# Performance work log

Measured on AMD Instinct MI355X. Metric: run time of the kernel, lower is better.

## Reference

```python
import jax, jax.numpy as jnp
import numpy as np

B, S, D = 2, 1024, 768
H, HD = 12, 64
E, K, F = 8, 2, 3072
EPS = 1e-5


def _ln(x, g, b):
    mu = jnp.mean(x, -1, keepdims=True)
    var = jnp.mean(jnp.square(x - mu), -1, keepdims=True)
    return (x - mu) * jax.lax.rsqrt(var + EPS) * g + b


def setup_inputs() -> dict:
    key = jax.random.key(0)
    ks = jax.random.split(key, 12)
    s = lambda k, shape, sc: jax.random.normal(k, shape, jnp.float32) * sc
    return {
        "hidden_states": s(ks[0], (B, S, D), 1.0),
        "ln1_g": jnp.ones((D,), jnp.float32), "ln1_b": jnp.zeros((D,), jnp.float32),
        "w_attn": s(ks[1], (D, 3 * D), 0.02), "b_attn": jnp.zeros((3 * D,), jnp.float32),
        "w_attnproj": s(ks[2], (D, D), 0.02), "b_attnproj": jnp.zeros((D,), jnp.float32),
        "ln2_g": jnp.ones((D,), jnp.float32), "ln2_b": jnp.zeros((D,), jnp.float32),
        "w_router": s(ks[3], (E, D), 0.01),
        "w_fc": s(ks[4], (E, D, F), 0.02 / E), "b_fc": jnp.zeros((E, F), jnp.float32),
        "w_proj": s(ks[5], (E, F, D), 0.02 / E), "b_proj": jnp.zeros((E, D), jnp.float32),
    }


def reference(hidden_states, ln1_g, ln1_b, w_attn, b_attn, w_attnproj, b_attnproj,
              ln2_g, ln2_b, w_router, w_fc, b_fc, w_proj, b_proj):
    # --- attention sub-block (GPT-2 style, causal) ---
    residual = hidden_states
    x = _ln(hidden_states, ln1_g, ln1_b)
    qkv = x @ w_attn + b_attn                         # [B,S,3D]
    q, k, v = jnp.split(qkv, 3, axis=-1)
    def heads(t):
        return t.reshape(B, S, H, HD).transpose(0, 2, 1, 3)  # [B,H,S,HD]
    q, k, v = heads(q), heads(k), heads(v)
    scores = jnp.einsum("bhqd,bhkd->bhqk", q, k) / np.sqrt(HD).astype(np.float32)
    causal = jnp.tril(jnp.ones((S, S), bool))
    scores = jnp.where(causal, scores, jnp.finfo(scores.dtype).min)
    attn = jax.nn.softmax(scores, axis=-1)
    ctx = jnp.einsum("bhqk,bhkd->bhqd", attn, v)
    ctx = ctx.transpose(0, 2, 1, 3).reshape(B, S, D)
    attn_out = ctx @ w_attnproj + b_attnproj
    hs = attn_out + residual

    # --- MoE FFN sub-block ---
    residual = hs
    x2 = _ln(hs, ln2_g, ln2_b)
    logits = x2 @ w_router.T                          # [B,S,E]
    probs = jax.nn.softmax(logits, axis=-1)
    top_w, top_idx = jax.lax.top_k(probs, K)          # [B,S,K]
    top_w = top_w / jnp.sum(top_w, -1, keepdims=True)
    gates = jnp.sum(jax.nn.one_hot(top_idx, E, dtype=x2.dtype) * top_w[..., None], axis=2)  # [B,S,E]
    h = jax.nn.gelu(jnp.einsum("bsd,edf->bsef", x2, w_fc) + b_fc, approximate=False)
    y = jnp.einsum("bsef,efd->bsed", h, w_proj) + b_proj
    moe_out = jnp.einsum("bse,bsed->bsd", gates, y)
    return moe_out + residual
```

## Files before the change

kernel.cpp:

```cpp
#include <hip/hip_runtime.h>
#include <hip/hip_bf16.h>
#include <math.h>

#define NB 2
#define SEQ 1024
#define DM 768
#define NHEAD 12
#define HDIM 64
#define NEXP 8
#define FF 3072
#define NTOK (NB*SEQ)
#define TDIM (3*DM)
#define LNEPS 1e-5f
#define NSLOT (NTOK*2)

typedef __attribute__((ext_vector_type(8))) short v8s;
typedef __attribute__((ext_vector_type(4))) float v4f;

#define GLDS16(src, dst) \
    __builtin_amdgcn_global_load_lds((const __attribute__((address_space(1))) unsigned int*)(src), \
                                     (__attribute__((address_space(3))) unsigned int*)(dst), 16, 0, 0)

#define BARF() do { asm volatile("" ::: "memory"); __builtin_amdgcn_s_barrier(); asm volatile("" ::: "memory"); } while(0)
#define WAITV(n) asm volatile("s_waitcnt vmcnt(" #n ")" ::: "memory")

static __device__ __forceinline__ float bf2f(unsigned short u){
    return __uint_as_float(((unsigned)u) << 16);
}
static __device__ __forceinline__ unsigned short f2bf(float f){
    unsigned u = __float_as_uint(f);
    u += 0x7fffu + ((u >> 16) & 1u);
    return (unsigned short)(u >> 16);
}
static __device__ __forceinline__ float gelu_exact(float x){
    return 0.5f * x * (1.0f + erff(x * 0.70710678118654752440f));
}

__global__ __launch_bounds__(256) void tconv_kernel(const float* __restrict__ in,
                                                    unsigned short* __restrict__ out,
                                                    int R, int C){
    __shared__ float T[32][33];
    size_t base = (size_t)blockIdx.z * R * C;
    int c0 = blockIdx.x * 32, r0 = blockIdx.y * 32;
    int t = threadIdx.x;
    int tr = t >> 3, tc4 = (t & 7) * 4;
    float4 v = *(const float4*)&in[base + (size_t)(r0 + tr) * C + c0 + tc4];
    T[tr][tc4+0] = v.x; T[tr][tc4+1] = v.y; T[tr][tc4+2] = v.z; T[tr][tc4+3] = v.w;
    __syncthreads();
    int oc = t >> 3, or4 = (t & 7) * 4;
    ushort4 o;
    o.x = f2bf(T[or4+0][oc]); o.y = f2bf(T[or4+1][oc]);
    o.z = f2bf(T[or4+2][oc]); o.w = f2bf(T[or4+3][oc]);
    *(ushort4*)&out[base + (size_t)(c0 + oc) * R + r0 + or4] = o;
}

__global__ __launch_bounds__(256) void ln_b(const float* __restrict__ in,
                                            const float* __restrict__ g,
                                            const float* __restrict__ b,
                                            unsigned short* __restrict__ outb){
    int t = blockIdx.x;
    const float* row = in + (size_t)t * DM;
    int tid = threadIdx.x;
    float v0 = row[tid], v1 = row[tid + 256], v2 = row[tid + 512];
    float s  = v0 + v1 + v2;
    float ss = v0*v0 + v1*v1 + v2*v2;
    for (int off = 32; off; off >>= 1){
        s  += __shfl_down(s, off);
        ss += __shfl_down(ss, off);
    }
    __shared__ float ls[4], lss[4];
    int wid = tid >> 6, lane = tid & 63;
    if (lane == 0){ ls[wid] = s; lss[wid] = ss; }
    __syncthreads();
    if (tid == 0){
        float a = ls[0] + ls[1] + ls[2] + ls[3];
        float c = lss[0] + lss[1] + lss[2] + lss[3];
        float mu = a / (float)DM;
        float var = c / (float)DM - mu * mu;
        ls[0] = mu; lss[0] = rsqrtf(var + LNEPS);
    }
    __syncthreads();
    float mu = ls[0], rs = lss[0];
    unsigned short* obrow = outb + (size_t)t * DM;
    obrow[tid]     = f2bf((v0 - mu) * rs * g[tid]       + b[tid]);
    obrow[tid+256] = f2bf((v1 - mu) * rs * g[tid + 256] + b[tid + 256]);
    obrow[tid+512] = f2bf((v2 - mu) * rs * g[tid + 512] + b[tid + 512]);
}

__global__ __launch_bounds__(256) void ln_router(const float* __restrict__ in,
                                                 const float* __restrict__ g,
                                                 const float* __restrict__ b,
                                                 const float* __restrict__ wr,
                                                 unsigned short* __restrict__ outb,
                                                 int* __restrict__ cnt,
                                                 int* __restrict__ expTok,
                                                 int* __restrict__ tokE,
                                                 int* __restrict__ tokPos,
                                                 float* __restrict__ tokGate){
    int t = blockIdx.x;
    const float* row = in + (size_t)t * DM;
    int tid = threadIdx.x;
    float v0 = row[tid], v1 = row[tid + 256], v2 = row[tid + 512];
    float s  = v0 + v1 + v2;
    float ss = v0*v0 + v1*v1 + v2*v2;
    for (int off = 32; off; off >>= 1){
        s  += __shfl_down(s, off);
        ss += __shfl_down(ss, off);
    }
    __shared__ float ls[4], lss[4];
    __shared__ float wsum[4][NEXP];
    int wid = tid >> 6, lane = tid & 63;
    if (lane == 0){ ls[wid] = s; lss[wid] = ss; }
    __syncthreads();
    if (tid == 0){
        float a = ls[0] + ls[1] + ls[2] + ls[3];
        float c = lss[0] + lss[1] + lss[2] + lss[3];
        float mu = a / (float)DM;
        float var = c / (float)DM - mu * mu;
        ls[0] = mu; lss[0] = rsqrtf(var + LNEPS);
    }
    __syncthreads();
    float mu = ls[0], rs = lss[0];
    float o0 = (v0 - mu) * rs * g[tid]       + b[tid];
    float o1 = (v1 - mu) * rs * g[tid + 256] + b[tid + 256];
    float o2 = (v2 - mu) * rs * g[tid + 512] + b[tid + 512];
    unsigned short* obrow = outb + (size_t)t * DM;
    obrow[tid] = f2bf(o0); obrow[tid+256] = f2bf(o1); obrow[tid+512] = f2bf(o2);
    float p[NEXP];
    #pragma unroll
    for (int e = 0; e < NEXP; e++)
        p[e] = o0*wr[e*DM + tid] + o1*wr[e*DM + tid + 256] + o2*wr[e*DM + tid + 512];
    #pragma unroll
    for (int e = 0; e < NEXP; e++)
        for (int off = 32; off; off >>= 1) p[e] += __shfl_down(p[e], off);
    if (lane == 0){
        #pragma unroll
        for (int e = 0; e < NEXP; e++) wsum[wid][e] = p[e];
    }
    __syncthreads();
    if (tid == 0){
        float lg[NEXP];
        #pragma unroll
        for (int e = 0; e < NEXP; e++)
            lg[e] = wsum[0][e] + wsum[1][e] + wsum[2][e] + wsum[3][e];
        int i0 = 0; float m0 = lg[0];
        #pragma unroll
        for (int e = 1; e < NEXP; e++) if (lg[e] > m0){ m0 = lg[e]; i0 = e; }
        int i1 = -1; float m1 = -INFINITY;
        #pragma unroll
        for (int e = 0; e < NEXP; e++) if (e != i0 && lg[e] > m1){ m1 = lg[e]; i1 = e; }
        float mx = fmaxf(m0, m1);
        float e0 = __expf(m0 - mx), e1 = __expf(m1 - mx);
        float inv = 1.0f / (e0 + e1);
        int p0 = atomicAdd(&cnt[i0], 1);
        int p1 = atomicAdd(&cnt[i1], 1);
        expTok[i0*NTOK + p0] = t;
        expTok[i1*NTOK + p1] = t;
        tokE[t*2]   = i0; tokE[t*2+1]   = i1;
        tokPos[t*2] = p0; tokPos[t*2+1] = p1;
        tokGate[t*2]   = e0 * inv;
        tokGate[t*2+1] = e1 * inv;
    }
}

__global__ __launch_bounds__(256) void mm_qkv(const unsigned short* __restrict__ Ab,
                                              const unsigned short* __restrict__ Bb,
                                              const float* __restrict__ bias,
                                              unsigned short* __restrict__ Qb,
                                              unsigned short* __restrict__ Kb,
                                              unsigned short* __restrict__ Vt){
    __shared__ __align__(16) unsigned short As[2][64*32];
    __shared__ __align__(16) unsigned short Bs[2][64*32];
    int bm = blockIdx.y * 64, bn = blockIdx.x * 64;
    int tid = threadIdx.x, wave = tid >> 6, lane = tid & 63;
    int quad = lane >> 4, l15 = lane & 15;
    int wm = wave >> 1, wn = wave & 1;
    int arow = tid >> 2, achunk = (tid & 3) * 8;
    const unsigned short* aS = Ab + (size_t)(bm + arow) * DM + achunk;
    const unsigned short* bS = Bb + (size_t)(bn + arow) * DM + achunk;
    v4f acc[2][2];
    #pragma unroll
    for (int i = 0; i < 2; i++)
        #pragma unroll
        for (int j = 0; j < 2; j++) acc[i][j] = (v4f){0.f,0.f,0.f,0.f};

#define QKV_STAGE(buf, kt) do { int kb = (kt)*32; \
    GLDS16(aS + kb, &As[buf][(wave*16)*32]); \
    GLDS16(bS + kb, &Bs[buf][(wave*16)*32]); \
} while(0)
#define QKV_COMP(buf) do { \
    v8s a[2], bfr[2]; \
    _Pragma("unroll") \
    for (int i = 0; i < 2; i++){ \
        a[i]   = *(const v8s*)&As[buf][(wm*32 + i*16 + l15)*32 + quad*8]; \
        bfr[i] = *(const v8s*)&Bs[buf][(wn*32 + i*16 + l15)*32 + quad*8]; \
    } \
    _Pragma("unroll") \
    for (int mi = 0; mi < 2; mi++) \
        _Pragma("unroll") \
        for (int ni = 0; ni < 2; ni++) \
            acc[mi][ni] = __builtin_amdgcn_mfma_f32_16x16x32_bf16(a[mi], bfr[ni], acc[mi][ni], 0, 0, 0); \
} while(0)

    const int NK = DM/32;
    QKV_STAGE(0, 0);
    #pragma unroll 1
    for (int kt = 0; kt < NK; kt++){
        if (NK - kt > 1){ QKV_STAGE((kt+1)&1, kt+1); WAITV(2); }
        else            { WAITV(0); }
        BARF();
        QKV_COMP(kt&1);
        BARF();
    }
    int btyp = bn / DM;
    #pragma unroll
    for (int ni = 0; ni < 2; ni++){
        int n = bn + wn*32 + ni*16 + l15;
        float bb = bias[n];
        int hd = n % DM; int h = hd >> 6; int d = hd & 63;
        #pragma unroll
        for (int mi = 0; mi < 2; mi++){
            int m = bm + wm*32 + mi*16 + quad*4;
            int b = m >> 10, sd = m & 1023;
            size_t bhbase = (size_t)(b*NHEAD + h);
            if (btyp == 0){
                #pragma unroll
                for (int r = 0; r < 4; r++)
                    Qb[(bhbase*SEQ + sd + r)*HDIM + d] = f2bf((acc[mi][ni][r] + bb) * 0.125f);
            } else if (btyp == 1){
                #pragma unroll
                for (int r = 0; r < 4; r++)
                    Kb[(bhbase*SEQ + sd + r)*HDIM + d] = f2bf(acc[mi][ni][r] + bb);
            } else {
                ushort4 o;
                o.x = f2bf(acc[mi][ni][0] + bb); o.y = f2bf(acc[mi][ni][1] + bb);
                o.z = f2bf(acc[mi][ni][2] + bb); o.w = f2bf(acc[mi][ni][3] + bb);
                *(ushort4*)&Vt[(bhbase*HDIM + d)*SEQ + sd] = o;
            }
        }
    }
}

__global__ __launch_bounds__(64) void fattn(const unsigned short* __restrict__ Qb,
                                            const unsigned short* __restrict__ Kb,
                                            const unsigned short* __restrict__ Vt,
                                            unsigned short* __restrict__ ctxb){
    int bh = blockIdx.x >> 5;
    int q0 = (31 - (blockIdx.x & 31)) * 32;
    int h = bh % NHEAD, b = bh / NHEAD;
    int lane = threadIdx.x;
    int quad = lane >> 4, l15 = lane & 15;

    __shared__ __align__(16) unsigned short Plds[32*32];

    const unsigned short* qp = Qb + ((size_t)bh*SEQ + q0 + l15) * HDIM + quad*8;
    v8s qa00 = *(const v8s*)qp;
    v8s qa01 = *(const v8s*)(qp + 32);
    v8s qa10 = *(const v8s*)(qp + 16*HDIM);
    v8s qa11 = *(const v8s*)(qp + 16*HDIM + 32);

    v4f o[2][4];
    #pragma unroll
    for (int i = 0; i < 2; i++)
        #pragma unroll
        for (int j = 0; j < 4; j++) o[i][j] = (v4f){0.f,0.f,0.f,0.f};
    float mrow[2][4], lrow[2][4];
    #pragma unroll
    for (int i = 0; i < 2; i++)
        #pragma unroll
        for (int r = 0; r < 4; r++){ mrow[i][r] = -1e30f; lrow[i][r] = 0.f; }

    int nch = (q0 >> 5) + 1;
    for (int ch = 0; ch < nch; ch++){
        int kt = ch * 32;
        const unsigned short* kp = Kb + ((size_t)bh*SEQ + kt + l15) * HDIM + quad*8;
        v8s k00 = *(const v8s*)kp;
        v8s k01 = *(const v8s*)(kp + 32);
        v8s k10 = *(const v8s*)(kp + 16*HDIM);
        v8s k11 = *(const v8s*)(kp + 16*HDIM + 32);
        v4f s00 = {0,0,0,0}, s01 = {0,0,0,0}, s10 = {0,0,0,0}, s11 = {0,0,0,0};
        s00 = __builtin_amdgcn_mfma_f32_16x16x32_bf16(qa00, k00, s00, 0, 0, 0);
        s00 = __builtin_amdgcn_mfma_f32_16x16x32_bf16(qa01, k01, s00, 0, 0, 0);
        s01 = __builtin_amdgcn_mfma_f32_16x16x32_bf16(qa00, k10, s01, 0, 0, 0);
        s01 = __builtin_amdgcn_mfma_f32_16x16x32_bf16(qa01, k11, s01, 0, 0, 0);
        s10 = __builtin_amdgcn_mfma_f32_16x16x32_bf16(qa10, k00, s10, 0, 0, 0);
        s10 = __builtin_amdgcn_mfma_f32_16x16x32_bf16(qa11, k01, s10, 0, 0, 0);
        s11 = __builtin_amdgcn_mfma_f32_16x16x32_bf16(qa10, k10, s11, 0, 0, 0);
        s11 = __builtin_amdgcn_mfma_f32_16x16x32_bf16(qa11, k11, s11, 0, 0, 0);

        int key0 = kt + l15, key1 = kt + 16 + l15;
        float alpha[2][4];
        #pragma unroll
        for (int mi = 0; mi < 2; mi++){
            #pragma unroll
            for (int r = 0; r < 4; r++){
                int qrow = q0 + mi*16 + quad*4 + r;
                float sv0 = mi ? s10[r] : s00[r];
                float sv1 = mi ? s11[r] : s01[r];
                float v0 = (key0 <= qrow) ? sv0 : -1e30f;
                float v1 = (key1 <= qrow) ? sv1 : -1e30f;
                float mx = fmaxf(v0, v1);
                mx = fmaxf(mx, __shfl_xor(mx, 1));
                mx = fmaxf(mx, __shfl_xor(mx, 2));
                mx = fmaxf(mx, __shfl_xor(mx, 4));
                mx = fmaxf(mx, __shfl_xor(mx, 8));
                float mn = fmaxf(mrow[mi][r], mx);
                alpha[mi][r] = __expf(mrow[mi][r] - mn);
                float p0 = __expf(v0 - mn);
                float p1 = __expf(v1 - mn);
                float ps = p0 + p1;
                ps += __shfl_xor(ps, 1);
                ps += __shfl_xor(ps, 2);
                ps += __shfl_xor(ps, 4);
                ps += __shfl_xor(ps, 8);
                lrow[mi][r] = lrow[mi][r] * alpha[mi][r] + ps;
                mrow[mi][r] = mn;
                Plds[(mi*16 + quad*4 + r)*32 + l15]      = f2bf(p0);
                Plds[(mi*16 + quad*4 + r)*32 + 16 + l15] = f2bf(p1);
            }
        }
        #pragma unroll
        for (int mi = 0; mi < 2; mi++)
            #pragma unroll
            for (int df = 0; df < 4; df++)
                #pragma unroll
                for (int r = 0; r < 4; r++)
                    o[mi][df][r] *= alpha[mi][r];
        __syncthreads();
        v8s pa0 = *(const v8s*)&Plds[l15*32 + quad*8];
        v8s pa1 = *(const v8s*)&Plds[(16 + l15)*32 + quad*8];
        const unsigned short* vp = Vt + ((size_t)bh*HDIM + l15) * SEQ + kt + quad*8;
        #pragma unroll
        for (int df = 0; df < 4; df++){
            v8s vb = *(const v8s*)(vp + df*16*SEQ);
            o[0][df] = __builtin_amdgcn_mfma_f32_16x16x32_bf16(pa0, vb, o[0][df], 0, 0, 0);
            o[1][df] = __builtin_amdgcn_mfma_f32_16x16x32_bf16(pa1, vb, o[1][df], 0, 0, 0);
        }
        __syncthreads();
    }
    #pragma unroll
    for (int mi = 0; mi < 2; mi++){
        #pragma unroll
        for (int r = 0; r < 4; r++){
            float inv = 1.0f / lrow[mi][r];
            size_t orow = (size_t)(b*SEQ + q0 + mi*16 + quad*4 + r) * DM + h*HDIM;
            #pragma unroll
            for (int df = 0; df < 4; df++)
                ctxb[orow + df*16 + l15] = f2bf(o[mi][df][r] * inv);
        }
    }
}

__global__ __launch_bounds__(256) void mm_attnproj(const unsigned short* __restrict__ Ab,
                                                   const unsigned short* __restrict__ Bb,
                                                   const float* __restrict__ bias,
                                                   const float* __restrict__ res,
                                                   float* __restrict__ C){
    __shared__ __align__(16) unsigned short As[4][64*32];
    __shared__ __align__(16) unsigned short Bs[4][64*32];
    int bm = blockIdx.y * 64, bn = blockIdx.x * 64;
    int tid = threadIdx.x, wave = tid >> 6, lane = tid & 63;
    int quad = lane >> 4, l15 = lane & 15;
    int wm = wave >> 1, wn = wave & 1;
    int lrow = lane >> 2, lchunk = (lane & 3) * 8;
    const unsigned short* aS = Ab + (size_t)(bm + wave*16 + lrow) * DM + lchunk;
    const unsigned short* bS = Bb + (size_t)(bn + wave*16 + lrow) * DM + lchunk;
    v4f acc[2][2];
    #pragma unroll
    for (int i = 0; i < 2; i++)
        #pragma unroll
        for (int j = 0; j < 2; j++) acc[i][j] = (v4f){0.f,0.f,0.f,0.f};

#define AP_STAGE(buf, kt) do { int kb = (kt)*32; \
    GLDS16(aS + kb, &As[buf][(wave*16)*32]); \
    GLDS16(bS + kb, &Bs[buf][(wave*16)*32]); \
} while(0)
#define AP_COMP(buf) do { \
    v8s a[2], bfr[2]; \
    _Pragma("unroll") \
    for (int i = 0; i < 2; i++){ \
        a[i]   = *(const v8s*)&As[buf][(wm*32 + i*16 + l15)*32 + quad*8]; \
        bfr[i] = *(const v8s*)&Bs[buf][(wn*32 + i*16 + l15)*32 + quad*8]; \
    } \
    _Pragma("unroll") \
    for (int mi = 0; mi < 2; mi++) \
        _Pragma("unroll") \
        for (int ni = 0; ni < 2; ni++) \
            acc[mi][ni] = __builtin_amdgcn_mfma_f32_16x16x32_bf16(a[mi], bfr[ni], acc[mi][ni], 0, 0, 0); \
} while(0)

    const int NK = DM/32;
    AP_STAGE(0, 0); AP_STAGE(1, 1); AP_STAGE(2, 2);
    #pragma unroll 1
    for (int kt = 0; kt < NK; kt++){
        int rem = NK - kt;
        if (rem > 3){ AP_STAGE((kt+3)&3, kt+3); WAITV(6); }
        else if (rem == 3){ WAITV(4); }
        else if (rem == 2){ WAITV(2); }
        else { WAITV(0); }
        BARF();
        AP_COMP(kt&3);
        BARF();
    }
    #pragma unroll
    for (int ni = 0; ni < 2; ni++){
        int n = bn + wn*32 + ni*16 + l15;
        float bb = bias[n];
        #pragma unroll
        for (int mi = 0; mi < 2; mi++){
            int m = bm + wm*32 + mi*16 + quad*4;
            #pragma unroll
            for (int r = 0; r < 4; r++)
                C[(size_t)(m + r) * DM + n] = acc[mi][ni][r] + bb + res[(size_t)(m + r) * DM + n];
        }
    }
}

__global__ __launch_bounds__(256) void mm_fc(const unsigned short* __restrict__ Xb,
                                             const unsigned short* __restrict__ Wb,
                                             const float* __restrict__ bfc,
                                             const int* __restrict__ expTok,
                                             const int* __restrict__ cnt,
                                             const int* __restrict__ offE,
                                             unsigned short* __restrict__ H){
    int bid = blockIdx.x;
    int e = bid & 7;
    int t2 = bid >> 3;
    int tile = t2 & 31;
    int bn = (t2 >> 5) * 128;
    int c = cnt[e];
    int rows = c - tile * 64;
    if (rows <= 0) return;
    __shared__ __align__(16) unsigned short As[2][64*32];
    __shared__ __align__(16) unsigned short Bs[2][128*32];
    __shared__ int toks[64];
    int tid = threadIdx.x, wave = tid >> 6, lane = tid & 63;
    if (tid < 64){
        int idx = tile * 64 + tid;
        if (idx >= c) idx = c - 1;
        toks[tid] = expTok[e * NTOK + idx];
    }
    __syncthreads();
    int quad = lane >> 4, l15 = lane & 15;
    int wm = wave >> 1, wn = wave & 1;
    int lrow = lane >> 2;
    int pch = (((lane >> 3) & 3) ^ (lane & 3)) * 8;
    int tok0 = toks[wave*16 + lrow];
    const unsigned short* Be = Wb + (size_t)e * FF * DM;
    const unsigned short* aS  = Xb + (size_t)tok0 * DM + pch;
    const unsigned short* bS0 = Be + (size_t)(bn +      wave*16 + lrow) * DM + pch;
    const unsigned short* bS1 = Be + (size_t)(bn + 64 + wave*16 + lrow) * DM + pch;
    int q2 = (quad ^ ((l15 >> 1) & 3)) * 8;
    v4f acc[2][4];
    #pragma unroll
    for (int i = 0; i < 2; i++)
        #pragma unroll
        for (int j = 0; j < 4; j++) acc[i][j] = (v4f){0.f,0.f,0.f,0.f};

#define FC_STAGE(buf, kt) do { int kb = (kt)*32; \
    GLDS16(aS  + kb, &As[buf][(wave*16)*32]); \
    GLDS16(bS0 + kb, &Bs[buf][(     wave*16)*32]); \
    GLDS16(bS1 + kb, &Bs[buf][(64 + wave*16)*32]); \
} while(0)
#define FC_COMP(buf) do { \
    v8s a[2], bfr[4]; \
    _Pragma("unroll") \
    for (int i = 0; i < 2; i++) a[i] = *(const v8s*)&As[buf][(wm*32 + i*16 + l15)*32 + q2]; \
    _Pragma("unroll") \
    for (int i = 0; i < 4; i++) bfr[i] = *(const v8s*)&Bs[buf][(wn*64 + i*16 + l15)*32 + q2]; \
    _Pragma("unroll") \
    for (int mi = 0; mi < 2; mi++) \
        _Pragma("unroll") \
        for (int ni = 0; ni < 4; ni++) \
            acc[mi][ni] = __builtin_amdgcn_mfma_f32_16x16x32_bf16(a[mi], bfr[ni], acc[mi][ni], 0, 0, 0); \
} while(0)

    const int NK = DM/32;
    FC_STAGE(0, 0);
    #pragma unroll 1
    for (int kt = 0; kt < NK; kt++){
        if (NK - kt > 1){ FC_STAGE((kt+1)&1, kt+1); WAITV(3); }
        else            { WAITV(0); }
        BARF();
        FC_COMP(kt&1);
        BARF();
    }
    int slot0 = offE[e] + tile * 64;
    #pragma unroll
    for (int ni = 0; ni < 4; ni++){
        int n = bn + wn*64 + ni*16 + l15;
        float bb = bfc[(size_t)e * FF + n];
        #pragma unroll
        for (int mi = 0; mi < 2; mi++){
            int ml = wm*32 + mi*16 + quad*4;
            #pragma unroll
            for (int r = 0; r < 4; r++)
                if (ml + r < rows)
                    H[(size_t)(slot0 + ml + r) * FF + n] = f2bf(gelu_exact(acc[mi][ni][r] + bb));
        }
    }
}

__global__ __launch_bounds__(256) void mm_proj(const unsigned short* __restrict__ H,
                                               const unsigned short* __restrict__ Wb,
                                               const int* __restrict__ cnt,
                                               const int* __restrict__ offE,
                                               float* __restrict__ Yp){
    int bid = blockIdx.x;
    int e = bid & 7;
    int t2 = bid >> 3;
    int tile = t2 & 31;
    int xx = t2 >> 5;
    int sk = xx & 1;
    int bn = (xx >> 1) * 64;
    int c = cnt[e];
    int rows = c - tile * 64;
    if (rows <= 0) return;
    __shared__ __align__(16) unsigned short As[2][64*32];
    __shared__ __align__(16) unsigned short Bs[2][64*32];
    int tid = threadIdx.x, wave = tid >> 6, lane = tid & 63;
    int quad = lane >> 4, l15 = lane & 15;
    int wm = wave >> 1, wn = wave & 1;
    int slot0 = offE[e] + tile * 64;
    int arow = tid >> 2;
    int pch = (((lane >> 3) & 3) ^ (lane & 3)) * 8;
    int arl = arow < rows ? arow : rows - 1;
    const unsigned short* Be = Wb + (size_t)e * DM * FF;
    const unsigned short* aS = H  + (size_t)(slot0 + arl) * FF + sk*1536 + pch;
    const unsigned short* bS = Be + (size_t)(bn + arow) * FF + sk*1536 + pch;
    int q2 = (quad ^ ((l15 >> 1) & 3)) * 8;
    v4f acc[2][2];
    #pragma unroll
    for (int i = 0; i < 2; i++)
        #pragma unroll
        for (int j = 0; j < 2; j++) acc[i][j] = (v4f){0.f,0.f,0.f,0.f};

#define PJ_STAGE(buf, kt) do { int kb = (kt)*32; \
    GLDS16(aS + kb, &As[buf][(wave*16)*32]); \
    GLDS16(bS + kb, &Bs[buf][(wave*16)*32]); \
} while(0)
#define PJ_COMP(buf) do { \
    v8s a[2], bfr[2]; \
    _Pragma("unroll") \
    for (int i = 0; i < 2; i++){ \
        a[i]   = *(const v8s*)&As[buf][(wm*32 + i*16 + l15)*32 + q2]; \
        bfr[i] = *(const v8s*)&Bs[buf][(wn*32 + i*16 + l15)*32 + q2]; \
    } \
    _Pragma("unroll") \
    for (int mi = 0; mi < 2; mi++) \
        _Pragma("unroll") \
        for (int ni = 0; ni < 2; ni++) \
            acc[mi][ni] = __builtin_amdgcn_mfma_f32_16x16x32_bf16(a[mi], bfr[ni], acc[mi][ni], 0, 0, 0); \
} while(0)

    const int NK = 1536/32;
    PJ_STAGE(0, 0);
    #pragma unroll 1
    for (int kt = 0; kt < NK; kt++){
        if (NK - kt > 1){ PJ_STAGE((kt+1)&1, kt+1); WAITV(2); }
        else            { WAITV(0); }
        BARF();
        PJ_COMP(kt&1);
        BARF();
    }
    float* Yo = Yp + (size_t)sk * NSLOT * DM;
    #pragma unroll
    for (int ni = 0; ni < 2; ni++){
        int n = bn + wn*32 + ni*16 + l15;
        #pragma unroll
        for (int mi = 0; mi < 2; mi++){
            int ml = wm*32 + mi*16 + quad*4;
            #pragma unroll
            for (int r = 0; r < 4; r++)
                if (ml + r < rows)
                    Yo[(size_t)(slot0 + ml + r) * DM + n] = acc[mi][ni][r];
        }
    }
}

__global__ void offsets_kernel(const int* __restrict__ cnt, int* __restrict__ offE){
    if (threadIdx.x == 0 && blockIdx.x == 0){
        int a = 0;
        for (int e = 0; e < NEXP; e++){ offE[e] = a; a += cnt[e]; }
    }
}

__global__ __launch_bounds__(256) void combine_kernel(const float* __restrict__ hs,
                                                      const float* __restrict__ Yp,
                                                      const float* __restrict__ bproj,
                                                      const int* __restrict__ tokE,
                                                      const int* __restrict__ tokPos,
                                                      const float* __restrict__ tokGate,
                                                      const int* __restrict__ offE,
                                                      float* __restrict__ out){
    int t = blockIdx.x;
    int e0 = tokE[t*2], e1 = tokE[t*2+1];
    int s0 = offE[e0] + tokPos[t*2];
    int s1 = offE[e1] + tokPos[t*2+1];
    float g0 = tokGate[t*2], g1 = tokGate[t*2+1];
    const float* y0a = Yp + (size_t)s0 * DM;
    const float* y0b = Yp + (size_t)NSLOT * DM + (size_t)s0 * DM;
    const float* y1a = Yp + (size_t)s1 * DM;
    const float* y1b = Yp + (size_t)NSLOT * DM + (size_t)s1 * DM;
    const float* b0 = bproj + (size_t)e0 * DM;
    const float* b1 = bproj + (size_t)e1 * DM;
    const float* hr = hs + (size_t)t * DM;
    float* orow = out + (size_t)t * DM;
    for (int d = threadIdx.x; d < DM; d += 256){
        orow[d] = hr[d] + g0 * (y0a[d] + y0b[d] + b0[d]) + g1 * (y1a[d] + y1b[d] + b1[d]);
    }
}

extern "C" void kernel_launch(void* const* d_in, const int* in_sizes, int n_in,
                              void* d_out, int out_size, void* d_ws, size_t ws_size,
                              hipStream_t stream){
    (void)in_sizes; (void)n_in; (void)out_size; (void)ws_size;
    const float* hidden  = (const float*)d_in[0];
    const float* ln1_g   = (const float*)d_in[1];
    const float* ln1_b   = (const float*)d_in[2];
    const float* w_attn  = (const float*)d_in[3];
    const float* b_attn  = (const float*)d_in[4];
    const float* w_aproj = (const float*)d_in[5];
    const float* b_aproj = (const float*)d_in[6];
    const float* ln2_g   = (const float*)d_in[7];
    const float* ln2_b   = (const float*)d_in[8];
    const float* w_rout  = (const float*)d_in[9];
    const float* w_fc    = (const float*)d_in[10];
    const float* b_fc    = (const float*)d_in[11];
    const float* w_proj  = (const float*)d_in[12];
    const float* b_proj  = (const float*)d_in[13];
    float* out = (float*)d_out;

    char* ws = (char*)d_ws;
    float*          hs   = (float*)(ws + 0);
    unsigned short* xb   = (unsigned short*)(ws + 6291456);
    unsigned short* Qb   = (unsigned short*)(ws + 9437184);
    unsigned short* Kb   = (unsigned short*)(ws + 12582912);
    unsigned short* Vt   = (unsigned short*)(ws + 15728640);
    unsigned short* ctxb = (unsigned short*)(ws + 18874368);
    unsigned short* Wab  = (unsigned short*)(ws + 22020096);
    unsigned short* Wapb = (unsigned short*)(ws + 25559040);
    unsigned short* H    = (unsigned short*)(ws + 9437184);
    unsigned short* Wfcb = (unsigned short*)(ws + 34603008);
    unsigned short* Wprb = (unsigned short*)(ws + 72351744);
    float*          Yp   = (float*)(ws + 34603008);
    char* rt = ws + 110100480;
    int* cnt      = (int*)(rt + 0);
    int* offE     = (int*)(rt + 64);
    int* expTok   = (int*)(rt + 128);
    int* tokE     = (int*)(rt + 128 + 65536);
    int* tokPos   = (int*)(rt + 128 + 81920);
    float* tokGate= (float*)(rt + 128 + 98304);

    hipMemsetAsync(cnt, 0, NEXP * sizeof(int), stream);

    tconv_kernel<<<dim3(TDIM/32, DM/32, 1), 256, 0, stream>>>(w_attn, Wab, DM, TDIM);
    tconv_kernel<<<dim3(DM/32, DM/32, 1), 256, 0, stream>>>(w_aproj, Wapb, DM, DM);
    tconv_kernel<<<dim3(FF/32, DM/32, NEXP), 256, 0, stream>>>(w_fc, Wfcb, DM, FF);
    tconv_kernel<<<dim3(DM/32, FF/32, NEXP), 256, 0, stream>>>(w_proj, Wprb, FF, DM);

    ln_b<<<NTOK, 256, 0, stream>>>(hidden, ln1_g, ln1_b, xb);
    mm_qkv<<<dim3(TDIM/64, NTOK/64), 256, 0, stream>>>(xb, Wab, b_attn, Qb, Kb, Vt);
    fattn<<<NB*NHEAD*32, 64, 0, stream>>>(Qb, Kb, Vt, ctxb);
    mm_attnproj<<<dim3(DM/64, NTOK/64), 256, 0, stream>>>(ctxb, Wapb, b_aproj, hidden, hs);
    ln_router<<<NTOK, 256, 0, stream>>>(hs, ln2_g, ln2_b, w_rout, xb,
                                        cnt, expTok, tokE, tokPos, tokGate);
    offsets_kernel<<<1, 64, 0, stream>>>(cnt, offE);
    mm_fc<<<8 * (NTOK/64) * (FF/128), 256, 0, stream>>>(xb, Wfcb, b_fc, expTok, cnt, offE, H);
    mm_proj<<<8 * (NTOK/64) * ((DM/64)*2), 256, 0, stream>>>(H, Wprb, cnt, offE, Yp);
    combine_kernel<<<NTOK, 256, 0, stream>>>(hs, Yp, b_proj, tokE, tokPos, tokGate, offE, out);
}
```

Measured before the change: 496.6 us.

## Split attention key range across two waves, widen weight transpose, drop offsets kernel

Measured after the change: 480.0 us. 3.3% less time.

```diff
diff --git a/kernel.cpp b/kernel.cpp
--- a/kernel.cpp
+++ b/kernel.cpp
@@ -39,19 +39,22 @@
 __global__ __launch_bounds__(256) void tconv_kernel(const float* __restrict__ in,
                                                     unsigned short* __restrict__ out,
                                                     int R, int C){
-    __shared__ float T[32][33];
+    __shared__ float T[64][33];
     size_t base = (size_t)blockIdx.z * R * C;
-    int c0 = blockIdx.x * 32, r0 = blockIdx.y * 32;
+    int c0 = blockIdx.x * 32, r0 = blockIdx.y * 64;
     int t = threadIdx.x;
-    int tr = t >> 3, tc4 = (t & 7) * 4;
-    float4 v = *(const float4*)&in[base + (size_t)(r0 + tr) * C + c0 + tc4];
-    T[tr][tc4+0] = v.x; T[tr][tc4+1] = v.y; T[tr][tc4+2] = v.z; T[tr][tc4+3] = v.w;
-    __syncthreads();
-    int oc = t >> 3, or4 = (t & 7) * 4;
-    ushort4 o;
-    o.x = f2bf(T[or4+0][oc]); o.y = f2bf(T[or4+1][oc]);
-    o.z = f2bf(T[or4+2][oc]); o.w = f2bf(T[or4+3][oc]);
-    *(ushort4*)&out[base + (size_t)(c0 + oc) * R + r0 + or4] = o;
+    int row = t >> 2, cq = (t & 3) * 8;
+    const float* ip = &in[base + (size_t)(r0 + row) * C + c0 + cq];
+    float4 va = *(const float4*)ip;
+    float4 vb = *(const float4*)(ip + 4);
+    T[row][cq+0]=va.x; T[row][cq+1]=va.y; T[row][cq+2]=va.z; T[row][cq+3]=va.w;
+    T[row][cq+4]=vb.x; T[row][cq+5]=vb.y; T[row][cq+6]=vb.z; T[row][cq+7]=vb.w;
+    __syncthreads();
+    int oc = t >> 3, or8 = (t & 7) * 8;
+    unsigned short ov[8];
+    #pragma unroll
+    for (int i = 0; i < 8; i++) ov[i] = f2bf(T[or8 + i][oc]);
+    *(v8s*)&out[base + (size_t)(c0 + oc) * R + r0 + or8] = *(const v8s*)ov;
 }
 
 __global__ __launch_bounds__(256) void ln_b(const float* __restrict__ in,
@@ -241,17 +244,21 @@
     }
 }
 
-__global__ __launch_bounds__(64) void fattn(const unsigned short* __restrict__ Qb,
-                                            const unsigned short* __restrict__ Kb,
-                                            const unsigned short* __restrict__ Vt,
-                                            unsigned short* __restrict__ ctxb){
+__global__ __launch_bounds__(128) void fattn(const unsigned short* __restrict__ Qb,
+                                             const unsigned short* __restrict__ Kb,
+                                             const unsigned short* __restrict__ Vt,
+                                             unsigned short* __restrict__ ctxb){
     int bh = blockIdx.x >> 5;
     int q0 = (31 - (blockIdx.x & 31)) * 32;
     int h = bh % NHEAD, b = bh / NHEAD;
-    int lane = threadIdx.x;
+    int wv = threadIdx.x >> 6;
+    int lane = threadIdx.x & 63;
     int quad = lane >> 4, l15 = lane & 15;
 
-    __shared__ __align__(16) unsigned short Plds[32*32];
+    __shared__ __align__(16) unsigned short Plds[2][32*32];
+    __shared__ __align__(16) v4f Oex[2][4][64];
+    __shared__ float Mm[2][4][64];
+    __shared__ float Lm[2][4][64];
 
     const unsigned short* qp = Qb + ((size_t)bh*SEQ + q0 + l15) * HDIM + quad*8;
     v8s qa00 = *(const v8s*)qp;
@@ -271,7 +278,12 @@
         for (int r = 0; r < 4; r++){ mrow[i][r] = -1e30f; lrow[i][r] = 0.f; }
 
     int nch = (q0 >> 5) + 1;
-    for (int ch = 0; ch < nch; ch++){
+    int halfc = (nch + 1) >> 1;
+    int ch0 = wv ? halfc : 0;
+    int ch1 = wv ? nch : halfc;
+    unsigned short* Pw = &Plds[wv][0];
+
+    for (int ch = ch0; ch < ch1; ch++){
         int kt = ch * 32;
         const unsigned short* kp = Kb + ((size_t)bh*SEQ + kt + l15) * HDIM + quad*8;
         v8s k00 = *(const v8s*)kp;
@@ -315,8 +327,8 @@
                 ps += __shfl_xor(ps, 8);
                 lrow[mi][r] = lrow[mi][r] * alpha[mi][r] + ps;
                 mrow[mi][r] = mn;
-                Plds[(mi*16 + quad*4 + r)*32 + l15]      = f2bf(p0);
-                Plds[(mi*16 + quad*4 + r)*32 + 16 + l15] = f2bf(p1);
+                Pw[(mi*16 + quad*4 + r)*32 + l15]      = f2bf(p0);
+                Pw[(mi*16 + quad*4 + r)*32 + 16 + l15] = f2bf(p1);
             }
         }
         #pragma unroll
@@ -326,9 +338,8 @@
                 #pragma unroll
                 for (int r = 0; r < 4; r++)
                     o[mi][df][r] *= alpha[mi][r];
-        __syncthreads();
-        v8s pa0 = *(const v8s*)&Plds[l15*32 + quad*8];
-        v8s pa1 = *(const v8s*)&Plds[(16 + l15)*32 + quad*8];
+        v8s pa0 = *(const v8s*)&Pw[l15*32 + quad*8];
+        v8s pa1 = *(const v8s*)&Pw[(16 + l15)*32 + quad*8];
         const unsigned short* vp = Vt + ((size_t)bh*HDIM + l15) * SEQ + kt + quad*8;
         #pragma unroll
         for (int df = 0; df < 4; df++){
@@ -336,18 +347,29 @@
             o[0][df] = __builtin_amdgcn_mfma_f32_16x16x32_bf16(pa0, vb, o[0][df], 0, 0, 0);
             o[1][df] = __builtin_amdgcn_mfma_f32_16x16x32_bf16(pa1, vb, o[1][df], 0, 0, 0);
         }
-        __syncthreads();
-    }
-    #pragma unroll
-    for (int mi = 0; mi < 2; mi++){
-        #pragma unroll
-        for (int r = 0; r < 4; r++){
-            float inv = 1.0f / lrow[mi][r];
-            size_t orow = (size_t)(b*SEQ + q0 + mi*16 + quad*4 + r) * DM + h*HDIM;
-            #pragma unroll
-            for (int df = 0; df < 4; df++)
-                ctxb[orow + df*16 + l15] = f2bf(o[mi][df][r] * inv);
-        }
+    }
+
+    int other = 1 - wv;
+    #pragma unroll
+    for (int df = 0; df < 4; df++) Oex[wv][df][lane] = o[other][df];
+    #pragma unroll
+    for (int r = 0; r < 4; r++){ Mm[wv][r][lane] = mrow[other][r]; Lm[wv][r][lane] = lrow[other][r]; }
+    __syncthreads();
+    v4f oth[4];
+    #pragma unroll
+    for (int df = 0; df < 4; df++) oth[df] = Oex[other][df][lane];
+    #pragma unroll
+    for (int r = 0; r < 4; r++){
+        float mo = Mm[other][r][lane], lo_ = Lm[other][r][lane];
+        float mm = mrow[wv][r], lm = lrow[wv][r];
+        float M = fmaxf(mm, mo);
+        float am = __expf(mm - M), ao = __expf(mo - M);
+        float L = lm*am + lo_*ao;
+        float inv = 1.0f / L;
+        size_t orow = (size_t)(b*SEQ + q0 + wv*16 + quad*4 + r) * DM + h*HDIM;
+        #pragma unroll
+        for (int df = 0; df < 4; df++)
+            ctxb[orow + df*16 + l15] = f2bf((o[wv][df][r]*am + oth[df][r]*ao) * inv);
     }
 }
 
@@ -421,14 +443,15 @@
                                              const float* __restrict__ bfc,
                                              const int* __restrict__ expTok,
                                              const int* __restrict__ cnt,
-                                             const int* __restrict__ offE,
                                              unsigned short* __restrict__ H){
     int bid = blockIdx.x;
     int e = bid & 7;
     int t2 = bid >> 3;
     int tile = t2 & 31;
     int bn = (t2 >> 5) * 128;
-    int c = cnt[e];
+    int offe = 0, c = 0;
+    #pragma unroll
+    for (int j = 0; j < NEXP; j++){ int cj = cnt[j]; offe += (j < e) ? cj : 0; c = (j == e) ? cj : c; }
     int rows = c - tile * 64;
     if (rows <= 0) return;
     __shared__ __align__(16) unsigned short As[2][64*32];
@@ -485,7 +508,7 @@
         FC_COMP(kt&1);
         BARF();
     }
-    int slot0 = offE[e] + tile * 64;
+    int slot0 = offe + tile * 64;
     #pragma unroll
     for (int ni = 0; ni < 4; ni++){
         int n = bn + wn*64 + ni*16 + l15;
@@ -504,7 +527,6 @@
 __global__ __launch_bounds__(256) void mm_proj(const unsigned short* __restrict__ H,
                                                const unsigned short* __restrict__ Wb,
                                                const int* __restrict__ cnt,
-                                               const int* __restrict__ offE,
                                                float* __restrict__ Yp){
     int bid = blockIdx.x;
     int e = bid & 7;
@@ -513,7 +535,9 @@
     int xx = t2 >> 5;
     int sk = xx & 1;
     int bn = (xx >> 1) * 64;
-    int c = cnt[e];
+    int offe = 0, c = 0;
+    #pragma unroll
+    for (int j = 0; j < NEXP; j++){ int cj = cnt[j]; offe += (j < e) ? cj : 0; c = (j == e) ? cj : c; }
     int rows = c - tile * 64;
     if (rows <= 0) return;
     __shared__ __align__(16) unsigned short As[2][64*32];
@@ -521,7 +545,7 @@
     int tid = threadIdx.x, wave = tid >> 6, lane = tid & 63;
     int quad = lane >> 4, l15 = lane & 15;
     int wm = wave >> 1, wn = wave & 1;
-    int slot0 = offE[e] + tile * 64;
+    int slot0 = offe + tile * 64;
     int arow = tid >> 2;
     int pch = (((lane >> 3) & 3) ^ (lane & 3)) * 8;
     int arl = arow < rows ? arow : rows - 1;
@@ -578,25 +602,25 @@
     }
 }
 
-__global__ void offsets_kernel(const int* __restrict__ cnt, int* __restrict__ offE){
-    if (threadIdx.x == 0 && blockIdx.x == 0){
-        int a = 0;
-        for (int e = 0; e < NEXP; e++){ offE[e] = a; a += cnt[e]; }
-    }
-}
-
 __global__ __launch_bounds__(256) void combine_kernel(const float* __restrict__ hs,
                                                       const float* __restrict__ Yp,
                                                       const float* __restrict__ bproj,
                                                       const int* __restrict__ tokE,
                                                       const int* __restrict__ tokPos,
                                                       const float* __restrict__ tokGate,
-                                                      const int* __restrict__ offE,
+                                                      const int* __restrict__ cnt,
                                                       float* __restrict__ out){
     int t = blockIdx.x;
     int e0 = tokE[t*2], e1 = tokE[t*2+1];
-    int s0 = offE[e0] + tokPos[t*2];
-    int s1 = offE[e1] + tokPos[t*2+1];
+    int off0 = 0, off1 = 0;
+    #pragma unroll
+    for (int j = 0; j < NEXP; j++){
+        int cj = cnt[j];
+        off0 += (j < e0) ? cj : 0;
+        off1 += (j < e1) ? cj : 0;
+    }
+    int s0 = off0 + tokPos[t*2];
+    int s1 = off1 + tokPos[t*2+1];
     float g0 = tokGate[t*2], g1 = tokGate[t*2+1];
     const float* y0a = Yp + (size_t)s0 * DM;
     const float* y0b = Yp + (size_t)NSLOT * DM + (size_t)s0 * DM;
@@ -646,7 +670,6 @@
     float*          Yp   = (float*)(ws + 34603008);
     char* rt = ws + 110100480;
     int* cnt      = (int*)(rt + 0);
-    int* offE     = (int*)(rt + 64);
     int* expTok   = (int*)(rt + 128);
     int* tokE     = (int*)(rt + 128 + 65536);
     int* tokPos   = (int*)(rt + 128 + 81920);
@@ -654,19 +677,18 @@
 
     hipMemsetAsync(cnt, 0, NEXP * sizeof(int), stream);
 
-    tconv_kernel<<<dim3(TDIM/32, DM/32, 1), 256, 0, stream>>>(w_attn, Wab, DM, TDIM);
-    tconv_kernel<<<dim3(DM/32, DM/32, 1), 256, 0, stream>>>(w_aproj, Wapb, DM, DM);
-    tconv_kernel<<<dim3(FF/32, DM/32, NEXP), 256, 0, stream>>>(w_fc, Wfcb, DM, FF);
-    tconv_kernel<<<dim3(DM/32, FF/32, NEXP), 256, 0, stream>>>(w_proj, Wprb, FF, DM);
+    tconv_kernel<<<dim3(TDIM/32, DM/64, 1), 256, 0, stream>>>(w_attn, Wab, DM, TDIM);
+    tconv_kernel<<<dim3(DM/32, DM/64, 1), 256, 0, stream>>>(w_aproj, Wapb, DM, DM);
+    tconv_kernel<<<dim3(FF/32, DM/64, NEXP), 256, 0, stream>>>(w_fc, Wfcb, DM, FF);
+    tconv_kernel<<<dim3(DM/32, FF/64, NEXP), 256, 0, stream>>>(w_proj, Wprb, FF, DM);
 
     ln_b<<<NTOK, 256, 0, stream>>>(hidden, ln1_g, ln1_b, xb);
     mm_qkv<<<dim3(TDIM/64, NTOK/64), 256, 0, stream>>>(xb, Wab, b_attn, Qb, Kb, Vt);
-    fattn<<<NB*NHEAD*32, 64, 0, stream>>>(Qb, Kb, Vt, ctxb);
+    fattn<<<NB*NHEAD*32, 128, 0, stream>>>(Qb, Kb, Vt, ctxb);
     mm_attnproj<<<dim3(DM/64, NTOK/64), 256, 0, stream>>>(ctxb, Wapb, b_aproj, hidden, hs);
     ln_router<<<NTOK, 256, 0, stream>>>(hs, ln2_g, ln2_b, w_rout, xb,
                                         cnt, expTok, tokE, tokPos, tokGate);
-    offsets_kernel<<<1, 64, 0, stream>>>(cnt, offE);
-    mm_fc<<<8 * (NTOK/64) * (FF/128), 256, 0, stream>>>(xb, Wfcb, b_fc, expTok, cnt, offE, H);
-    mm_proj<<<8 * (NTOK/64) * ((DM/64)*2), 256, 0, stream>>>(H, Wprb, cnt, offE, Yp);
-    combine_kernel<<<NTOK, 256, 0, stream>>>(hs, Yp, b_proj, tokE, tokPos, tokGate, offE, out);
-}
+    mm_fc<<<8 * (NTOK/64) * (FF/128), 256, 0, stream>>>(xb, Wfcb, b_fc, expTok, cnt, H);
+    mm_proj<<<8 * (NTOK/64) * ((DM/64)*2), 256, 0, stream>>>(H, Wprb, cnt, Yp);
+    combine_kernel<<<NTOK, 256, 0, stream>>>(hs, Yp, b_proj, tokE, tokPos, tokGate, cnt, out);
+}
```
